# Optimization experiments

Hardware: AMD Instinct MI355X
Metric: run time of the kernel (lower is better)

Reference implementation:

```python
import jax, jax.numpy as jnp
import numpy as np

NUM_CLASSES = 10
ALPHA = 0.25
GAMMA = 2.0
BETA = 1.0
EPS = 1e-7


def _corners(centers, dims, yaws):
    # centers [N,2], dims [N,2] (l,w), yaws [N] -> corners [N,4,2]
    half = dims * 0.5
    base = jnp.array([[1., 1.], [-1., 1.], [-1., -1.], [1., -1.]], dtype=centers.dtype)
    base = base[None, :, :] * half[:, None, :]  # [N,4,2]
    c, s = jnp.cos(yaws), jnp.sin(yaws)
    x = base[..., 0] * c[:, None] - base[..., 1] * s[:, None]
    y = base[..., 0] * s[:, None] + base[..., 1] * c[:, None]
    corners = jnp.stack([x, y], axis=-1) + centers[:, None, :]
    return corners[:, jnp.array([3, 2, 1, 0]), :]  # reorder as in torch code


def _cross(u, v):
    return u[..., 0] * v[..., 1] - u[..., 1] * v[..., 0]


def _signed_area(q):  # q [...,4,2]
    return 0.5 * jnp.sum(_cross(q, jnp.roll(q, -1, axis=-2)), axis=-1)


def _pts_in_quad(pts, quad, sgn):
    # pts [N,P,2] inside convex quad [N,4,2]; sgn = orientation sign of quad [N]
    a = quad
    e = jnp.roll(quad, -1, axis=-2) - a  # [N,4,2]
    d = pts[:, :, None, :] - a[:, None, :, :]  # [N,P,4,2]
    cr = e[:, None, :, 0] * d[..., 1] - e[:, None, :, 1] * d[..., 0]  # [N,P,4]
    return jnp.all(cr * sgn[:, None, None] >= -1e-9, axis=-1)


def _rotated_iou(cA, cB):
    # Exact convex-quad intersection IoU (replaces the per-box Shapely loop).
    N = cA.shape[0]
    sgnA = jnp.sign(_signed_area(cA))
    sgnB = jnp.sign(_signed_area(cB))
    vA_in_B = _pts_in_quad(cA, cB, sgnB)  # [N,4]
    vB_in_A = _pts_in_quad(cB, cA, sgnA)  # [N,4]
    # all 4x4 edge-edge intersections
    a1 = cA; a2 = jnp.roll(cA, -1, axis=1)
    b1 = cB; b2 = jnp.roll(cB, -1, axis=1)
    da = (a2 - a1)[:, :, None, :]  # [N,4,1,2]
    db = (b2 - b1)[:, None, :, :]  # [N,1,4,2]
    dp = b1[:, None, :, :] - a1[:, :, None, :]  # [N,4,4,2]
    den = _cross(da, db)  # [N,4,4]
    den_safe = jnp.where(jnp.abs(den) < 1e-12, 1.0, den)
    t = _cross(dp, db) / den_safe
    s = _cross(dp, da) / den_safe
    val_x = (jnp.abs(den) > 1e-12) & (t >= 0) & (t <= 1) & (s >= 0) & (s <= 1)
    xpts = a1[:, :, None, :] + t[..., None] * da  # [N,4,4,2]
    # up to 24 candidate vertices of the convex intersection polygon
    pts = jnp.concatenate([cA, cB, xpts.reshape(N, 16, 2)], axis=1)  # [N,24,2]
    valid = jnp.concatenate([vA_in_B, vB_in_A, val_x.reshape(N, 16)], axis=1)
    pts = jnp.where(valid[..., None], pts, 0.0)
    nv = valid.sum(axis=1)
    cent = pts.sum(axis=1) / jnp.maximum(nv, 1)[:, None]
    ang = jnp.arctan2(pts[..., 1] - cent[:, None, 1], pts[..., 0] - cent[:, None, 0])
    key = jnp.where(valid, ang, 1e9)
    order = jnp.argsort(key, axis=1)
    ps = jnp.take_along_axis(pts, order[..., None], axis=1)
    vs = jnp.take_along_axis(valid, order, axis=1)
    ps = jnp.where(vs[..., None], ps, ps[:, :1, :])  # pad with first valid vertex
    inter = 0.5 * jnp.abs(jnp.sum(_cross(ps, jnp.roll(ps, -1, axis=1)), axis=1))
    inter = jnp.where(nv >= 3, inter, 0.0)
    areaA = jnp.abs(_signed_area(cA))
    areaB = jnp.abs(_signed_area(cB))
    union = areaA + areaB - inter
    return jnp.where(union > 1e-7, inter / union, 0.0)


def _sl1(p, t):
    d = jnp.abs(p - t)
    return jnp.where(d < BETA, 0.5 * d * d / BETA, d - 0.5 * BETA)


def setup_inputs() -> dict:
    key = jax.random.key(0)
    ks = jax.random.split(key, 7)
    B, C, H, W = 8, NUM_CLASSES, 256, 256
    cls_pred = jax.random.normal(ks[0], (B, C, H, W), dtype=jnp.float32)
    reg_pred = jax.random.uniform(ks[1], (B, 9, H, W), dtype=jnp.float32)
    iou_pred = jax.random.normal(ks[2], (B, 1, H, W), dtype=jnp.float32)
    cls_targets = jax.random.randint(ks[3], (B, H, W), 0, C, dtype=jnp.int32)
    reg_targets = jax.random.uniform(ks[4], (B, 9, H, W), dtype=jnp.float32)
    reg_weights = jax.random.randint(ks[5], (B, H, W), 0, 2).astype(jnp.float32)
    iou_targets = jax.random.uniform(ks[6], (B, 1, H, W), dtype=jnp.float32)
    return {"cls_pred": cls_pred, "reg_pred": reg_pred, "iou_pred": iou_pred,
            "cls_targets": cls_targets, "reg_targets": reg_targets,
            "reg_weights": reg_weights, "iou_targets": iou_targets}


def reference(cls_pred, reg_pred, iou_pred, cls_targets, reg_targets, reg_weights, iou_targets):
    B, C, H, W = cls_pred.shape
    N = B * H * W
    clsf = jnp.transpose(cls_pred, (0, 2, 3, 1)).reshape(N, C)
    regf = jnp.transpose(reg_pred, (0, 2, 3, 1)).reshape(N, 9)
    regt = jnp.transpose(reg_targets, (0, 2, 3, 1)).reshape(N, 9)
    iouf = jnp.transpose(iou_pred, (0, 2, 3, 1)).reshape(N)
    iout = iou_targets.reshape(N)
    ct = cls_targets.reshape(N)
    w = reg_weights.reshape(N)
    pos = (w > 0).astype(clsf.dtype)
    num_pos = jnp.maximum(pos.sum(), 1.0)
    # focal classification loss
    valid = ct >= 0
    p = jax.nn.softmax(clsf, axis=1)
    tl = jnp.clip(ct, 0, C - 1)
    pt = jnp.clip(jnp.take_along_axis(p, tl[:, None], axis=1)[:, 0], EPS, 1.0 - EPS)
    alpha_t = jnp.where(ct > 0, ALPHA, 1.0 - ALPHA)
    fl = -alpha_t * (1.0 - pt) ** GAMMA * jnp.log(pt)
    cls_loss = jnp.sum(jnp.where(valid, fl, 0.0)) / num_pos
    cen_p, dim_p, yaw_p = regf[:, :2], regf[:, 3:5], regf[:, 6]
    cen_t, dim_t, yaw_t = regt[:, :2], regt[:, 3:5], regt[:, 6]
    cp = _corners(cen_p, dim_p, yaw_p)
    ctg = _corners(cen_t, dim_t, yaw_t)
    iou = jax.lax.stop_gradient(_rotated_iou(cp, ctg))
    d2 = jnp.sum((cen_p - cen_t) ** 2, axis=-1)
    allc = jnp.concatenate([cp, ctg], axis=1)  # [N,8,2]
    c2 = jnp.maximum(jnp.sum((allc.max(axis=1) - allc.min(axis=1)) ** 2, axis=-1), EPS)
    loss_bev = 1.0 - iou + d2 / c2
    at_p = jnp.arctan(dim_p[:, 1] / jnp.maximum(dim_p[:, 0], EPS))
    at_t = jnp.arctan(dim_t[:, 1] / jnp.maximum(dim_t[:, 0], EPS))
    v = (4.0 / np.pi ** 2) * (at_p - at_t) ** 2
    alpha_c = jax.lax.stop_gradient(v / (1.0 - iou + v + EPS))
    loss_bev = loss_bev + alpha_c * v
    bev_loss = jnp.sum(loss_bev * pos) / num_pos
    # smooth-L1 terms: z (ch 2), h (ch 5), vel (ch 7:9)
    z_loss = jnp.sum(_sl1(regf[:, 2], regt[:, 2]) * pos) / num_pos
    h_loss = jnp.sum(_sl1(regf[:, 5], regt[:, 5]) * pos) / num_pos
    vel_loss = jnp.sum(_sl1(regf[:, 7:9], regt[:, 7:9]).sum(axis=-1) * pos) / num_pos
    # BCE-with-logits IoU head loss
    x, y = iouf, iout
    bce = jnp.maximum(x, 0.0) - x * y + jnp.log1p(jnp.exp(-jnp.abs(x)))
    iou_loss = jnp.sum(bce * pos) / num_pos
    return jnp.stack([cls_loss, bev_loss, z_loss, h_loss, vel_loss, iou_loss])
```

## Files before the change

kernel.cpp:

```cpp
#include <hip/hip_runtime.h>
#include <cstdint>
#include <cstddef>

#define B_ 8
#define C_ 10
#define HW_ 65536
#define NPIX_ (B_ * HW_)

__device__ __forceinline__ float sl1f(float p, float t) {
    float d = fabsf(p - t);
    return (d < 1.0f) ? 0.5f * d * d : d - 0.5f;
}

__device__ __forceinline__ void pixel_loss(
    const float lg[C_], int ct, const float P[9], const float T[9],
    float w, float xiou, float yiou, float o[7])
{
    float m = lg[0];
    #pragma unroll
    for (int c = 1; c < C_; c++) m = fmaxf(m, lg[c]);
    float se = 0.f;
    float ex[C_];
    #pragma unroll
    for (int c = 0; c < C_; c++) { ex[c] = __expf(lg[c] - m); se += ex[c]; }
    int tl = ct < 0 ? 0 : (ct > C_ - 1 ? C_ - 1 : ct);
    float et = 0.f;
    #pragma unroll
    for (int c = 0; c < C_; c++) et = (c == tl) ? ex[c] : et;
    float pt = __fdividef(et, se);
    pt = fminf(fmaxf(pt, 1e-7f), 1.0f - 1e-7f);
    float alpha_t = (ct > 0) ? 0.25f : 0.75f;
    float omp = 1.0f - pt;
    float fl = -alpha_t * omp * omp * __logf(pt);
    o[0] = (ct >= 0) ? fl : 0.0f;

    float pos = (w > 0.f) ? 1.f : 0.f;

    float Ax[4], Ay[4], Bx[4], By[4];
    {
        const float sbx[4] = { 1.f, -1.f, -1.f, 1.f };
        const float sby[4] = { -1.f, -1.f, 1.f, 1.f };
        float hx = 0.5f * P[3], hy = 0.5f * P[4];
        float ss, cc; __sincosf(P[6], &ss, &cc);
        #pragma unroll
        for (int i = 0; i < 4; i++) {
            float px = sbx[i] * hx, py = sby[i] * hy;
            Ax[i] = px * cc - py * ss + P[0];
            Ay[i] = px * ss + py * cc + P[1];
        }
        float hx2 = 0.5f * T[3], hy2 = 0.5f * T[4];
        float ss2, cc2; __sincosf(T[6], &ss2, &cc2);
        #pragma unroll
        for (int i = 0; i < 4; i++) {
            float px = sbx[i] * hx2, py = sby[i] * hy2;
            Bx[i] = px * cc2 - py * ss2 + T[0];
            By[i] = px * ss2 + py * cc2 + T[1];
        }
    }

    float sa = 0.f, sb = 0.f;
    #pragma unroll
    for (int i = 0; i < 4; i++) {
        int j = (i + 1) & 3;
        sa += Ax[i] * Ay[j] - Ay[i] * Ax[j];
        sb += Bx[i] * By[j] - By[i] * Bx[j];
    }
    sa *= 0.5f; sb *= 0.5f;
    float sgnA = (sa > 0.f) ? 1.f : ((sa < 0.f) ? -1.f : 0.f);
    float sgnB = (sb > 0.f) ? 1.f : ((sb < 0.f) ? -1.f : 0.f);

    float dB[4][4], dA[4][4];
    #pragma unroll
    for (int j = 0; j < 4; j++) {
        int j1 = (j + 1) & 3;
        float ex_ = Bx[j1] - Bx[j], ey_ = By[j1] - By[j];
        #pragma unroll
        for (int i = 0; i < 4; i++)
            dB[j][i] = sgnB * (ex_ * (Ay[i] - By[j]) - ey_ * (Ax[i] - Bx[j]));
    }
    #pragma unroll
    for (int j = 0; j < 4; j++) {
        int j1 = (j + 1) & 3;
        float ex_ = Ax[j1] - Ax[j], ey_ = Ay[j1] - Ay[j];
        #pragma unroll
        for (int i = 0; i < 4; i++)
            dA[j][i] = sgnA * (ex_ * (By[i] - Ay[j]) - ey_ * (Bx[i] - Ax[j]));
    }

    float S = 0.f;
    #pragma unroll
    for (int i = 0; i < 4; i++) {
        int i1 = (i + 1) & 3;
        float t0 = 0.f, t1 = 1.f;
        #pragma unroll
        for (int j = 0; j < 4; j++) {
            float d0 = dB[j][i], d1 = dB[j][i1];
            float den = d1 - d0;
            float t = __fdividef(-d0, den);
            if (den > 0.f)       t0 = fmaxf(t0, t);
            else if (den < 0.f)  t1 = fminf(t1, t);
            else if (d0 < 0.f)   t0 = 2.f;
        }
        S += (Ax[i] * Ay[i1] - Ay[i] * Ax[i1]) * fmaxf(t1 - t0, 0.f);
    }
    #pragma unroll
    for (int i = 0; i < 4; i++) {
        int i1 = (i + 1) & 3;
        float t0 = 0.f, t1 = 1.f;
        #pragma unroll
        for (int j = 0; j < 4; j++) {
            float d0 = dA[j][i], d1 = dA[j][i1];
            float den = d1 - d0;
            float t = __fdividef(-d0, den);
            if (den > 0.f)       t0 = fmaxf(t0, t);
            else if (den < 0.f)  t1 = fminf(t1, t);
            else if (d0 < 0.f)   t0 = 2.f;
        }
        S += (Bx[i] * By[i1] - By[i] * Bx[i1]) * fmaxf(t1 - t0, 0.f);
    }
    float inter = 0.5f * fabsf(S);

    float areaA = fabsf(sa), areaB = fabsf(sb);
    float uni = areaA + areaB - inter;
    float iou = (uni > 1e-7f) ? __fdividef(inter, uni) : 0.f;

    float ddx = P[0] - T[0], ddy = P[1] - T[1];
    float d2 = ddx * ddx + ddy * ddy;
    float mnx = Ax[0], mxx = Ax[0], mny = Ay[0], mxy = Ay[0];
    #pragma unroll
    for (int i = 1; i < 4; i++) {
        mnx = fminf(mnx, Ax[i]); mxx = fmaxf(mxx, Ax[i]);
        mny = fminf(mny, Ay[i]); mxy = fmaxf(mxy, Ay[i]);
    }
    #pragma unroll
    for (int i = 0; i < 4; i++) {
        mnx = fminf(mnx, Bx[i]); mxx = fmaxf(mxx, Bx[i]);
        mny = fminf(mny, By[i]); mxy = fmaxf(mxy, By[i]);
    }
    float exd = mxx - mnx, eyd = mxy - mny;
    float c2 = fmaxf(exd * exd + eyd * eyd, 1e-7f);

    float atp = atanf(__fdividef(P[4], fmaxf(P[3], 1e-7f)));
    float att = atanf(__fdividef(T[4], fmaxf(T[3], 1e-7f)));
    float dv = atp - att;
    float v = 0.4052847345693511f * dv * dv;
    float alpha_c = __fdividef(v, 1.0f - iou + v + 1e-7f);
    float lbev = 1.0f - iou + __fdividef(d2, c2) + alpha_c * v;
    o[1] = lbev * pos;

    o[2] = sl1f(P[2], T[2]) * pos;
    o[3] = sl1f(P[5], T[5]) * pos;
    o[4] = (sl1f(P[7], T[7]) + sl1f(P[8], T[8])) * pos;

    float bce = fmaxf(xiou, 0.f) - xiou * yiou + __logf(1.0f + __expf(-fabsf(xiou)));
    o[5] = bce * pos;
    o[6] = pos;
}

__global__ __launch_bounds__(256) void bev_loss_main(
    const float* __restrict__ cls_pred, const float* __restrict__ reg_pred,
    const float* __restrict__ iou_pred, const int* __restrict__ cls_tg,
    const float* __restrict__ reg_tg, const float* __restrict__ reg_w,
    const float* __restrict__ iou_tg, double* __restrict__ part)
{
    int t  = blockIdx.x * blockDim.x + threadIdx.x;
    int n0 = t << 1;
    int b  = n0 >> 16;
    int hw = n0 & 65535;

    float2 lg2[C_];
    {
        const float* cp = cls_pred + (size_t)b * C_ * HW_ + hw;
        #pragma unroll
        for (int c = 0; c < C_; c++)
            lg2[c] = *reinterpret_cast<const float2*>(cp + (size_t)c * HW_);
    }
    float2 P2[9], T2[9];
    {
        const float* rp = reg_pred + (size_t)b * 9 * HW_ + hw;
        const float* rt = reg_tg  + (size_t)b * 9 * HW_ + hw;
        #pragma unroll
        for (int k = 0; k < 9; k++) {
            P2[k] = *reinterpret_cast<const float2*>(rp + (size_t)k * HW_);
            T2[k] = *reinterpret_cast<const float2*>(rt + (size_t)k * HW_);
        }
    }
    int2   ct2 = *reinterpret_cast<const int2*>(cls_tg + n0);
    float2 w2  = *reinterpret_cast<const float2*>(reg_w + n0);
    float2 x2  = *reinterpret_cast<const float2*>(iou_pred + n0);
    float2 y2  = *reinterpret_cast<const float2*>(iou_tg + n0);

    float o0[7], o1[7];
    {
        float lg[C_], P[9], T[9];
        #pragma unroll
        for (int c = 0; c < C_; c++) lg[c] = lg2[c].x;
        #pragma unroll
        for (int k = 0; k < 9; k++) { P[k] = P2[k].x; T[k] = T2[k].x; }
        pixel_loss(lg, ct2.x, P, T, w2.x, x2.x, y2.x, o0);
    }
    {
        float lg[C_], P[9], T[9];
        #pragma unroll
        for (int c = 0; c < C_; c++) lg[c] = lg2[c].y;
        #pragma unroll
        for (int k = 0; k < 9; k++) { P[k] = P2[k].y; T[k] = T2[k].y; }
        pixel_loss(lg, ct2.y, P, T, w2.y, x2.y, y2.y, o1);
    }

    __shared__ double red[4][7];
    int lane = threadIdx.x & 63;
    int wv   = threadIdx.x >> 6;
    #pragma unroll
    for (int k = 0; k < 7; k++) {
        double s = (double)o0[k] + (double)o1[k];
        for (int off = 32; off > 0; off >>= 1) s += __shfl_down(s, off, 64);
        if (lane == 0) red[wv][k] = s;
    }
    __syncthreads();
    if (threadIdx.x == 0) {
        #pragma unroll
        for (int k = 0; k < 7; k++)
            part[(size_t)blockIdx.x * 7 + k] = red[0][k] + red[1][k] + red[2][k] + red[3][k];
    }
}

__global__ void bev_loss_fin(const double* __restrict__ part, float* __restrict__ out, int nb) {
    int l = threadIdx.x;
    double s[7] = { 0, 0, 0, 0, 0, 0, 0 };
    for (int i = l; i < nb; i += 64) {
        #pragma unroll
        for (int k = 0; k < 7; k++) s[k] += part[(size_t)i * 7 + k];
    }
    #pragma unroll
    for (int k = 0; k < 7; k++) {
        for (int off = 32; off > 0; off >>= 1) s[k] += __shfl_down(s[k], off, 64);
    }
    if (l == 0) {
        double npos = fmax(s[6], 1.0);
        #pragma unroll
        for (int k = 0; k < 6; k++) out[k] = (float)(s[k] / npos);
    }
}

extern "C" void kernel_launch(void* const* d_in, const int* in_sizes, int n_in,
                              void* d_out, int out_size, void* d_ws, size_t ws_size,
                              hipStream_t stream) {
    const float* cls_pred = (const float*)d_in[0];
    const float* reg_pred = (const float*)d_in[1];
    const float* iou_pred = (const float*)d_in[2];
    const int*   cls_tg   = (const int*)d_in[3];
    const float* reg_tg   = (const float*)d_in[4];
    const float* reg_w    = (const float*)d_in[5];
    const float* iou_tg   = (const float*)d_in[6];
    float* out = (float*)d_out;
    double* part = (double*)d_ws;

    const int nb = 1024;
    bev_loss_main<<<nb, 256, 0, stream>>>(cls_pred, reg_pred, iou_pred, cls_tg,
                                          reg_tg, reg_w, iou_tg, part);
    bev_loss_fin<<<1, 64, 0, stream>>>(part, out, nb);
}
```

Before: 37.77 us.

## Pin loads early, streamline IoU clipping math, and widen final reduction

Empty inline-asm register pins are placed on every loaded value so the compiler issues all global loads before the compute. The clipping code becomes branchless, computes edge distances with a hoisted constant per edge, and scopes each half so fewer registers are live at once. The two arctans are merged into one via the arctan difference identity, and the softmax loop is fused. The final reduction kernel now uses 1024 threads over a transposed partials layout instead of one 64-thread wave striding the data. The arctan identity breaks when rp*rt < -1, which may change results for negative dimensions, and the pins may raise register pressure.

```diff
diff --git a/kernel.cpp b/kernel.cpp
--- a/kernel.cpp
+++ b/kernel.cpp
@@ -6,11 +6,14 @@
 #define C_ 10
 #define HW_ 65536
 #define NPIX_ (B_ * HW_)
+#define NB_ 1024
 
 __device__ __forceinline__ float sl1f(float p, float t) {
     float d = fabsf(p - t);
     return (d < 1.0f) ? 0.5f * d * d : d - 0.5f;
 }
+__device__ __forceinline__ void pinf(float v)  { asm volatile("" :: "v"(v)); }
+__device__ __forceinline__ void pini(int v)    { asm volatile("" :: "v"(v)); }
 
 __device__ __forceinline__ void pixel_loss(
     const float lg[C_], int ct, const float P[9], const float T[9],
@@ -19,14 +22,14 @@
     float m = lg[0];
     #pragma unroll
     for (int c = 1; c < C_; c++) m = fmaxf(m, lg[c]);
-    float se = 0.f;
-    float ex[C_];
-    #pragma unroll
-    for (int c = 0; c < C_; c++) { ex[c] = __expf(lg[c] - m); se += ex[c]; }
     int tl = ct < 0 ? 0 : (ct > C_ - 1 ? C_ - 1 : ct);
-    float et = 0.f;
-    #pragma unroll
-    for (int c = 0; c < C_; c++) et = (c == tl) ? ex[c] : et;
+    float se = 0.f, et = 0.f;
+    #pragma unroll
+    for (int c = 0; c < C_; c++) {
+        float e = __expf(lg[c] - m);
+        se += e;
+        et = (c == tl) ? e : et;
+    }
     float pt = __fdividef(et, se);
     pt = fminf(fmaxf(pt, 1e-7f), 1.0f - 1e-7f);
     float alpha_t = (ct > 0) ? 0.25f : 0.75f;
@@ -69,89 +72,99 @@
     float sgnA = (sa > 0.f) ? 1.f : ((sa < 0.f) ? -1.f : 0.f);
     float sgnB = (sb > 0.f) ? 1.f : ((sb < 0.f) ? -1.f : 0.f);
 
-    float dB[4][4], dA[4][4];
-    #pragma unroll
-    for (int j = 0; j < 4; j++) {
-        int j1 = (j + 1) & 3;
-        float ex_ = Bx[j1] - Bx[j], ey_ = By[j1] - By[j];
-        #pragma unroll
-        for (int i = 0; i < 4; i++)
-            dB[j][i] = sgnB * (ex_ * (Ay[i] - By[j]) - ey_ * (Ax[i] - Bx[j]));
-    }
-    #pragma unroll
-    for (int j = 0; j < 4; j++) {
-        int j1 = (j + 1) & 3;
-        float ex_ = Ax[j1] - Ax[j], ey_ = Ay[j1] - Ay[j];
-        #pragma unroll
-        for (int i = 0; i < 4; i++)
-            dA[j][i] = sgnA * (ex_ * (By[i] - Ay[j]) - ey_ * (Bx[i] - Ax[j]));
-    }
-
     float S = 0.f;
-    #pragma unroll
-    for (int i = 0; i < 4; i++) {
-        int i1 = (i + 1) & 3;
-        float t0 = 0.f, t1 = 1.f;
+    {
+        float dB[4][4];
         #pragma unroll
         for (int j = 0; j < 4; j++) {
-            float d0 = dB[j][i], d1 = dB[j][i1];
-            float den = d1 - d0;
-            float t = __fdividef(-d0, den);
-            if (den > 0.f)       t0 = fmaxf(t0, t);
-            else if (den < 0.f)  t1 = fminf(t1, t);
-            else if (d0 < 0.f)   t0 = 2.f;
-        }
-        S += (Ax[i] * Ay[i1] - Ay[i] * Ax[i1]) * fmaxf(t1 - t0, 0.f);
-    }
-    #pragma unroll
-    for (int i = 0; i < 4; i++) {
-        int i1 = (i + 1) & 3;
-        float t0 = 0.f, t1 = 1.f;
+            int j1 = (j + 1) & 3;
+            float sx = sgnB * (Bx[j1] - Bx[j]);
+            float sy = sgnB * (By[j1] - By[j]);
+            float kj = sx * By[j] - sy * Bx[j];
+            #pragma unroll
+            for (int i = 0; i < 4; i++)
+                dB[j][i] = sx * Ay[i] - sy * Ax[i] - kj;
+        }
+        #pragma unroll
+        for (int i = 0; i < 4; i++) {
+            int i1 = (i + 1) & 3;
+            float t0 = 0.f, t1 = 1.f;
+            #pragma unroll
+            for (int j = 0; j < 4; j++) {
+                float d0 = dB[j][i], d1 = dB[j][i1];
+                float den = d1 - d0;
+                float t = __fdividef(-d0, den);
+                float lo = (den > 0.f) ? t : ((den == 0.f && d0 < 0.f) ? 2.f : 0.f);
+                float hi = (den < 0.f) ? t : 1.f;
+                t0 = fmaxf(t0, lo);
+                t1 = fminf(t1, hi);
+            }
+            S += (Ax[i] * Ay[i1] - Ay[i] * Ax[i1]) * fmaxf(t1 - t0, 0.f);
+        }
+    }
+    {
+        float dA[4][4];
         #pragma unroll
         for (int j = 0; j < 4; j++) {
-            float d0 = dA[j][i], d1 = dA[j][i1];
-            float den = d1 - d0;
-            float t = __fdividef(-d0, den);
-            if (den > 0.f)       t0 = fmaxf(t0, t);
-            else if (den < 0.f)  t1 = fminf(t1, t);
-            else if (d0 < 0.f)   t0 = 2.f;
-        }
-        S += (Bx[i] * By[i1] - By[i] * Bx[i1]) * fmaxf(t1 - t0, 0.f);
+            int j1 = (j + 1) & 3;
+            float sx = sgnA * (Ax[j1] - Ax[j]);
+            float sy = sgnA * (Ay[j1] - Ay[j]);
+            float kj = sx * Ay[j] - sy * Ax[j];
+            #pragma unroll
+            for (int i = 0; i < 4; i++)
+                dA[j][i] = sx * By[i] - sy * Bx[i] - kj;
+        }
+        #pragma unroll
+        for (int i = 0; i < 4; i++) {
+            int i1 = (i + 1) & 3;
+            float t0 = 0.f, t1 = 1.f;
+            #pragma unroll
+            for (int j = 0; j < 4; j++) {
+                float d0 = dA[j][i], d1 = dA[j][i1];
+                float den = d1 - d0;
+                float t = __fdividef(-d0, den);
+                float lo = (den > 0.f) ? t : ((den == 0.f && d0 < 0.f) ? 2.f : 0.f);
+                float hi = (den < 0.f) ? t : 1.f;
+                t0 = fmaxf(t0, lo);
+                t1 = fminf(t1, hi);
+            }
+            S += (Bx[i] * By[i1] - By[i] * Bx[i1]) * fmaxf(t1 - t0, 0.f);
+        }
     }
     float inter = 0.5f * fabsf(S);
-
     float areaA = fabsf(sa), areaB = fabsf(sb);
     float uni = areaA + areaB - inter;
     float iou = (uni > 1e-7f) ? __fdividef(inter, uni) : 0.f;
 
-    float ddx = P[0] - T[0], ddy = P[1] - T[1];
-    float d2 = ddx * ddx + ddy * ddy;
-    float mnx = Ax[0], mxx = Ax[0], mny = Ay[0], mxy = Ay[0];
-    #pragma unroll
-    for (int i = 1; i < 4; i++) {
-        mnx = fminf(mnx, Ax[i]); mxx = fmaxf(mxx, Ax[i]);
-        mny = fminf(mny, Ay[i]); mxy = fmaxf(mxy, Ay[i]);
-    }
-    #pragma unroll
-    for (int i = 0; i < 4; i++) {
-        mnx = fminf(mnx, Bx[i]); mxx = fmaxf(mxx, Bx[i]);
-        mny = fminf(mny, By[i]); mxy = fmaxf(mxy, By[i]);
-    }
-    float exd = mxx - mnx, eyd = mxy - mny;
-    float c2 = fmaxf(exd * exd + eyd * eyd, 1e-7f);
-
-    float atp = atanf(__fdividef(P[4], fmaxf(P[3], 1e-7f)));
-    float att = atanf(__fdividef(T[4], fmaxf(T[3], 1e-7f)));
-    float dv = atp - att;
-    float v = 0.4052847345693511f * dv * dv;
-    float alpha_c = __fdividef(v, 1.0f - iou + v + 1e-7f);
-    float lbev = 1.0f - iou + __fdividef(d2, c2) + alpha_c * v;
-    o[1] = lbev * pos;
+    {
+        float ddx = P[0] - T[0], ddy = P[1] - T[1];
+        float d2 = fmaf(ddx, ddx, ddy * ddy);
+        float mnx = Ax[0], mxx = Ax[0], mny = Ay[0], mxy = Ay[0];
+        #pragma unroll
+        for (int i = 1; i < 4; i++) {
+            mnx = fminf(mnx, Ax[i]); mxx = fmaxf(mxx, Ax[i]);
+            mny = fminf(mny, Ay[i]); mxy = fmaxf(mxy, Ay[i]);
+        }
+        #pragma unroll
+        for (int i = 0; i < 4; i++) {
+            mnx = fminf(mnx, Bx[i]); mxx = fmaxf(mxx, Bx[i]);
+            mny = fminf(mny, By[i]); mxy = fmaxf(mxy, By[i]);
+        }
+        float exd = mxx - mnx, eyd = mxy - mny;
+        float c2 = fmaxf(fmaf(exd, exd, eyd * eyd), 1e-7f);
+
+        float rp = __fdividef(P[4], fmaxf(P[3], 1e-7f));
+        float rt = __fdividef(T[4], fmaxf(T[3], 1e-7f));
+        float dv = atanf(__fdividef(rp - rt, fmaf(rp, rt, 1.f)));
+        float v = 0.4052847345693511f * dv * dv;
+        float alpha_c = __fdividef(v, 1.0f - iou + v + 1e-7f);
+        float lbev = 1.0f - iou + __fdividef(d2, c2) + alpha_c * v;
+        o[1] = lbev * pos;
+    }
 
     o[2] = sl1f(P[2], T[2]) * pos;
     o[3] = sl1f(P[5], T[5]) * pos;
     o[4] = (sl1f(P[7], T[7]) + sl1f(P[8], T[8])) * pos;
-
     float bce = fmaxf(xiou, 0.f) - xiou * yiou + __logf(1.0f + __expf(-fabsf(xiou)));
     o[5] = bce * pos;
     o[6] = pos;
@@ -190,6 +203,15 @@
     float2 x2  = *reinterpret_cast<const float2*>(iou_pred + n0);
     float2 y2  = *reinterpret_cast<const float2*>(iou_tg + n0);
 
+    #pragma unroll
+    for (int c = 0; c < C_; c++) { pinf(lg2[c].x); pinf(lg2[c].y); }
+    #pragma unroll
+    for (int k = 0; k < 9; k++) { pinf(P2[k].x); pinf(P2[k].y); pinf(T2[k].x); pinf(T2[k].y); }
+    pini(ct2.x); pini(ct2.y);
+    pinf(w2.x);  pinf(w2.y);
+    pinf(x2.x);  pinf(x2.y);
+    pinf(y2.x);  pinf(y2.y);
+
     float o0[7], o1[7];
     {
         float lg[C_], P[9], T[9];
@@ -208,38 +230,52 @@
         pixel_loss(lg, ct2.y, P, T, w2.y, x2.y, y2.y, o1);
     }
 
-    __shared__ double red[4][7];
+    __shared__ double red[7][4];
     int lane = threadIdx.x & 63;
     int wv   = threadIdx.x >> 6;
     #pragma unroll
     for (int k = 0; k < 7; k++) {
         double s = (double)o0[k] + (double)o1[k];
         for (int off = 32; off > 0; off >>= 1) s += __shfl_down(s, off, 64);
-        if (lane == 0) red[wv][k] = s;
+        if (lane == 0) red[k][wv] = s;
     }
     __syncthreads();
     if (threadIdx.x == 0) {
         #pragma unroll
         for (int k = 0; k < 7; k++)
-            part[(size_t)blockIdx.x * 7 + k] = red[0][k] + red[1][k] + red[2][k] + red[3][k];
-    }
-}
-
-__global__ void bev_loss_fin(const double* __restrict__ part, float* __restrict__ out, int nb) {
-    int l = threadIdx.x;
-    double s[7] = { 0, 0, 0, 0, 0, 0, 0 };
-    for (int i = l; i < nb; i += 64) {
-        #pragma unroll
-        for (int k = 0; k < 7; k++) s[k] += part[(size_t)i * 7 + k];
-    }
+            part[(size_t)k * NB_ + blockIdx.x] = red[k][0] + red[k][1] + red[k][2] + red[k][3];
+    }
+}
+
+__global__ __launch_bounds__(1024) void bev_loss_fin(
+    const double* __restrict__ part, float* __restrict__ out)
+{
+    int t = threadIdx.x;
+    double v[7];
+    #pragma unroll
+    for (int k = 0; k < 7; k++) v[k] = part[(size_t)k * NB_ + t];
+
+    int lane = t & 63, wv = t >> 6;
+    __shared__ double red[7][16];
     #pragma unroll
     for (int k = 0; k < 7; k++) {
-        for (int off = 32; off > 0; off >>= 1) s[k] += __shfl_down(s[k], off, 64);
-    }
-    if (l == 0) {
-        double npos = fmax(s[6], 1.0);
-        #pragma unroll
-        for (int k = 0; k < 6; k++) out[k] = (float)(s[k] / npos);
+        double s = v[k];
+        for (int off = 32; off > 0; off >>= 1) s += __shfl_down(s, off, 64);
+        if (lane == 0) red[k][wv] = s;
+    }
+    __syncthreads();
+    if (t == 0) {
+        double tot[7];
+        #pragma unroll
+        for (int k = 0; k < 7; k++) {
+            double s = 0.0;
+            #pragma unroll
+            for (int i = 0; i < 16; i++) s += red[k][i];
+            tot[k] = s;
+        }
+        double npos = fmax(tot[6], 1.0);
+        #pragma unroll
+        for (int k = 0; k < 6; k++) out[k] = (float)(tot[k] / npos);
     }
 }
 
@@ -256,8 +292,7 @@
     float* out = (float*)d_out;
     double* part = (double*)d_ws;
 
-    const int nb = 1024;
-    bev_loss_main<<<nb, 256, 0, stream>>>(cls_pred, reg_pred, iou_pred, cls_tg,
-                                          reg_tg, reg_w, iou_tg, part);
-    bev_loss_fin<<<1, 64, 0, stream>>>(part, out, nb);
-}
+    bev_loss_main<<<NB_, 256, 0, stream>>>(cls_pred, reg_pred, iou_pred, cls_tg,
+                                           reg_tg, reg_w, iou_tg, part);
+    bev_loss_fin<<<1, 1024, 0, stream>>>(part, out);
+}
```

New measurement: 35.46 us. 1.07x faster.
